# Optimization experiments

Measured on AMD Instinct MI355X. Metric: run time of the kernel, lower is better.

The kernel has to match this reference:

```python
import jax, jax.numpy as jnp
import numpy as np

B, TV, TH, F, H, D = 16, 128, 64, 512, 512, 256


def setup_inputs() -> dict:
    key = jax.random.key(0)
    ks = jax.random.split(key, 6)
    return {
        "v": jax.random.normal(ks[0], (B, TV, F), dtype=jnp.float32),
        "h": jax.random.normal(ks[1], (B, TH, H), dtype=jnp.float32),
        "W": jax.random.normal(ks[2], (F, D), dtype=jnp.float32) * 0.05,
        "U": jax.random.normal(ks[3], (H, D), dtype=jnp.float32) * 0.05,
        "b": jax.random.normal(ks[4], (D,), dtype=jnp.float32) * 0.05,
        "w": jax.random.normal(ks[5], (D, 1), dtype=jnp.float32) * 0.05,
    }


def reference(v, h, W, U, b, w):
    # v: [B, Tv, F] video features; h: [B, Th, H] decoder hidden states
    Wv = jnp.einsum("btf,fd->btd", v, W)      # [B, Tv, D]
    Uh = jnp.einsum("bsh,hd->bsd", h, U)      # [B, Th, D]
    # Broadcast add -> [B, Th, Tv, D], tanh nonlinearity (additive attention)
    f = jnp.tanh(Uh[:, :, None, :] + Wv[:, None, :, :] + b)
    q = jnp.einsum("bstd,d->bst", f, w[:, 0])  # scores [B, Th, Tv]
    beta = jax.nn.softmax(q, axis=-1)           # softmax over Tv (axis -2 of q[..., None])
    u = jnp.einsum("bst,btf->bsf", beta, v)    # context [B, Th, F]
    return u
```

## Files before the change

### kernel.cpp

```cpp
#include <hip/hip_runtime.h>
#include <hip/hip_bf16.h>

#define BB 16
#define TV 128
#define TH 64
#define FF 512
#define HH 512
#define DD 256

#define LOG2E2 2.8853900817779268f

typedef __attribute__((ext_vector_type(8))) short bf16x8;
typedef __attribute__((ext_vector_type(4))) float f32x4;

__device__ __forceinline__ float fast_exp2(float x) {
#if __has_builtin(__builtin_amdgcn_exp2f)
  return __builtin_amdgcn_exp2f(x);
#else
  return __expf(x * 0.6931471805599453f);
#endif
}
__device__ __forceinline__ float fast_rcp(float x) {
#if __has_builtin(__builtin_amdgcn_rcpf)
  return __builtin_amdgcn_rcpf(x);
#else
  return 1.0f / x;
#endif
}
__device__ __forceinline__ unsigned short f2bf(float x) {
  union { float f; unsigned u; } a; a.f = x;
  unsigned r = a.u + 0x7fffu + ((a.u >> 16) & 1u);
  return (unsigned short)(r >> 16);
}

#define NT_V 262144
#define NT_H 131072
#define NT_W 32768
__global__ __launch_bounds__(256) void convert_kernel(
    const float* __restrict__ v, const float* __restrict__ h,
    const float* __restrict__ W, const float* __restrict__ U,
    unsigned short* __restrict__ vb, unsigned short* __restrict__ hb,
    unsigned short* __restrict__ WT, unsigned short* __restrict__ UT) {
  int task = blockIdx.x * 256 + threadIdx.x;
  if (task < NT_V) {
    float4 x = ((const float4*)v)[task];
    ushort4 o = make_ushort4(f2bf(x.x), f2bf(x.y), f2bf(x.z), f2bf(x.w));
    *(ushort4*)&vb[(size_t)task * 4] = o;
  } else if (task < NT_V + NT_H) {
    int t2 = task - NT_V;
    float4 x = ((const float4*)h)[t2];
    ushort4 o = make_ushort4(f2bf(x.x), f2bf(x.y), f2bf(x.z), f2bf(x.w));
    *(ushort4*)&hb[(size_t)t2 * 4] = o;
  } else {
    int t2 = task - NT_V - NT_H;
    const float* S;
    unsigned short* Dt;
    if (t2 < NT_W) { S = W; Dt = WT; } else { S = U; Dt = UT; t2 -= NT_W; }
    int n = t2 & 255, k4 = t2 >> 8;
    float a0 = S[(k4 * 4 + 0) * 256 + n];
    float a1 = S[(k4 * 4 + 1) * 256 + n];
    float a2 = S[(k4 * 4 + 2) * 256 + n];
    float a3 = S[(k4 * 4 + 3) * 256 + n];
    ushort4 o = make_ushort4(f2bf(a0), f2bf(a1), f2bf(a2), f2bf(a3));
    *(ushort4*)&Dt[(size_t)n * 512 + k4 * 4] = o;
  }
}

__global__ __launch_bounds__(128) void mfma_gemm_kernel(
    const unsigned short* __restrict__ Av, const unsigned short* __restrict__ Ah,
    const unsigned short* __restrict__ WT, const unsigned short* __restrict__ UT,
    const float* __restrict__ bias, float* __restrict__ EaT,
    float* __restrict__ EuhT) {
  const int bid = blockIdx.x;
  const unsigned short* A;
  const unsigned short* BT;
  int mt, nt;
  bool is_wv;
  if (bid < 256) {
    A = Av; BT = WT; is_wv = true;
    mt = bid >> 3; nt = bid & 7;
  } else {
    const int b2 = bid - 256;
    A = Ah; BT = UT; is_wv = false;
    mt = b2 >> 3; nt = b2 & 7;
  }
  const int wv   = threadIdx.x >> 6;
  const int lane = threadIdx.x & 63;
  const int m0   = mt * 64 + wv * 32;
  const int n0   = nt * 32;
  const int r16  = lane & 15;
  const int quad = lane >> 4;

  const unsigned short* a0p = A + (size_t)(m0 + r16) * 512 + quad * 8;
  const unsigned short* a1p = a0p + 16 * 512;
  const unsigned short* b0p = BT + (size_t)(n0 + r16) * 512 + quad * 8;
  const unsigned short* b1p = b0p + 16 * 512;

  f32x4 acc00 = {0.f, 0.f, 0.f, 0.f};
  f32x4 acc01 = {0.f, 0.f, 0.f, 0.f};
  f32x4 acc10 = {0.f, 0.f, 0.f, 0.f};
  f32x4 acc11 = {0.f, 0.f, 0.f, 0.f};

#pragma unroll
  for (int kc = 0; kc < 16; kc++) {
    bf16x8 a0 = *(const bf16x8*)(a0p + kc * 32);
    bf16x8 a1 = *(const bf16x8*)(a1p + kc * 32);
    bf16x8 b0 = *(const bf16x8*)(b0p + kc * 32);
    bf16x8 b1 = *(const bf16x8*)(b1p + kc * 32);
    acc00 = __builtin_amdgcn_mfma_f32_16x16x32_bf16(a0, b0, acc00, 0, 0, 0);
    acc01 = __builtin_amdgcn_mfma_f32_16x16x32_bf16(a0, b1, acc01, 0, 0, 0);
    acc10 = __builtin_amdgcn_mfma_f32_16x16x32_bf16(a1, b0, acc10, 0, 0, 0);
    acc11 = __builtin_amdgcn_mfma_f32_16x16x32_bf16(a1, b1, acc11, 0, 0, 0);
  }

  if (is_wv) {
    const int bb   = m0 >> 7;
    const int tb   = (m0 & 127) + quad * 4;
    float* Wb = EaT + (size_t)bb * 32768;
#pragma unroll
    for (int r = 0; r < 4; r++) {
      Wb[(size_t)(n0 + r16) * 128 + tb + r]           = fast_exp2(acc00[r] * LOG2E2);
      Wb[(size_t)(n0 + 16 + r16) * 128 + tb + r]      = fast_exp2(acc01[r] * LOG2E2);
      Wb[(size_t)(n0 + r16) * 128 + tb + 16 + r]      = fast_exp2(acc10[r] * LOG2E2);
      Wb[(size_t)(n0 + 16 + r16) * 128 + tb + 16 + r] = fast_exp2(acc11[r] * LOG2E2);
    }
  } else {
    const float bj0 = bias[n0 + r16];
    const float bj1 = bias[n0 + 16 + r16];
#pragma unroll
    for (int r = 0; r < 4; r++) {
      const int row0 = m0 + quad * 4 + r;
      EuhT[(size_t)row0 * 256 + n0 + r16]             = fast_exp2((acc00[r] + bj0) * LOG2E2);
      EuhT[(size_t)row0 * 256 + n0 + 16 + r16]        = fast_exp2((acc01[r] + bj1) * LOG2E2);
      EuhT[(size_t)(row0 + 16) * 256 + n0 + r16]      = fast_exp2((acc10[r] + bj0) * LOG2E2);
      EuhT[(size_t)(row0 + 16) * 256 + n0 + 16 + r16] = fast_exp2((acc11[r] + bj1) * LOG2E2);
    }
  }
}

__global__ __launch_bounds__(1024) void attn_fused_kernel(
    const float* __restrict__ EaT, const float* __restrict__ EuhT,
    const float* __restrict__ wg, const float* __restrict__ v,
    float* __restrict__ u) {
  __shared__ float EuhS[4 * 256];
  __shared__ float wS[256];
  __shared__ float pS[4 * 16 * 128];
  __shared__ float bS[4 * 128];
  __shared__ float mW[8];
  __shared__ float sW[8];

  const int tid = threadIdx.x;
  const int bid  = blockIdx.x;
  const int slot = bid >> 3;
  const int b    = (bid & 7) * 2 + (slot >> 4);
  const int sg   = slot & 15;
  const int s0   = sg * 4;

  if (tid < 256) {
    const int row = tid >> 6, q4 = (tid & 63) << 2;
    *(float4*)&EuhS[row * 256 + q4] =
        *(const float4*)&EuhT[(size_t)(b * 64 + s0 + row) * 256 + q4];
  } else if (tid < 320) {
    const int q4 = (tid - 256) << 2;
    *(float4*)&wS[q4] = *(const float4*)&wg[q4];
  }
  __syncthreads();

  {
    const int t4  = tid & 31;
    const int dgf = tid >> 5;
    const float* eab = EaT + (size_t)b * 32768 + (size_t)dgf * 8 * 128 + t4 * 4;

    float eu[4][8];
    float wr[8];
#pragma unroll
    for (int s = 0; s < 4; s++) {
      *(float4*)&eu[s][0] = *(const float4*)&EuhS[s * 256 + dgf * 8];
      *(float4*)&eu[s][4] = *(const float4*)&EuhS[s * 256 + dgf * 8 + 4];
    }
    *(float4*)&wr[0] = *(const float4*)&wS[dgf * 8];
    *(float4*)&wr[4] = *(const float4*)&wS[dgf * 8 + 4];

    f32x4 acc[4];
#pragma unroll
    for (int s = 0; s < 4; s++) acc[s] = (f32x4){0.f, 0.f, 0.f, 0.f};

#pragma unroll
    for (int jp = 0; jp < 4; jp++) {
      float4 e0 = *(const float4*)(eab + (2 * jp + 0) * 128);
      float4 e1 = *(const float4*)(eab + (2 * jp + 1) * 128);
      const float w0 = wr[2 * jp], w1 = wr[2 * jp + 1];
#pragma unroll
      for (int s = 0; s < 4; s++) {
        const float u0 = eu[s][2 * jp], u1 = eu[s][2 * jp + 1];
        float D0, D1, num;
        D0 = fmaf(e0.x, u0, 1.0f); D1 = fmaf(e1.x, u1, 1.0f);
        num = fmaf(w1, D0, w0 * D1);
        acc[s][0] = fmaf(num, fast_rcp(D0 * D1), acc[s][0]);
        D0 = fmaf(e0.y, u0, 1.0f); D1 = fmaf(e1.y, u1, 1.0f);
        num = fmaf(w1, D0, w0 * D1);
        acc[s][1] = fmaf(num, fast_rcp(D0 * D1), acc[s][1]);
        D0 = fmaf(e0.z, u0, 1.0f); D1 = fmaf(e1.z, u1, 1.0f);
        num = fmaf(w1, D0, w0 * D1);
        acc[s][2] = fmaf(num, fast_rcp(D0 * D1), acc[s][2]);
        D0 = fmaf(e0.w, u0, 1.0f); D1 = fmaf(e1.w, u1, 1.0f);
        num = fmaf(w1, D0, w0 * D1);
        acc[s][3] = fmaf(num, fast_rcp(D0 * D1), acc[s][3]);
      }
    }

#pragma unroll
    for (int s = 0; s < 4; s++) {
#pragma unroll
      for (int c = 0; c < 4; c++) acc[s][c] += __shfl_xor(acc[s][c], 32, 64);
    }
    const int wv_ = tid >> 6;
    if ((tid & 63) < 32) {
#pragma unroll
      for (int s = 0; s < 4; s++) {
        float4 o = make_float4(acc[s][0], acc[s][1], acc[s][2], acc[s][3]);
        *(float4*)&pS[(s * 16 + wv_) * 128 + t4 * 4] = o;
      }
    }
  }
  __syncthreads();

  float qv = 0.0f, ev = 0.0f;
  const int wvid = tid >> 6, lane = tid & 63;
  if (tid < 512) {
    const int s_l = tid >> 7, t = tid & 127;
    float ssum = 0.0f;
#pragma unroll
    for (int k = 0; k < 16; k++) ssum += pS[(s_l * 16 + k) * 128 + t];
    qv = ssum * (-LOG2E2);
    float m = qv;
#pragma unroll
    for (int off = 32; off > 0; off >>= 1) m = fmaxf(m, __shfl_xor(m, off, 64));
    if (lane == 0) mW[wvid] = m;
  }
  __syncthreads();
  if (tid < 512) {
    float m = fmaxf(mW[wvid], mW[wvid ^ 1]);
    ev = fast_exp2(qv - m);
    float ssum = ev;
#pragma unroll
    for (int off = 32; off > 0; off >>= 1) ssum += __shfl_xor(ssum, off, 64);
    if (lane == 0) sW[wvid] = ssum;
  }
  __syncthreads();
  if (tid < 512) {
    const int s_l = tid >> 7, t = tid & 127;
    bS[s_l * 128 + t] = ev * fast_rcp(sW[wvid] + sW[wvid ^ 1]);
  }
  __syncthreads();

  const float* vb2 = v + (size_t)b * TV * FF;
  const int f  = tid & 511;
  const int sh = tid >> 9;
  float a0 = 0.f, a1 = 0.f;
#pragma unroll 4
  for (int tg = 0; tg < 128; tg += 4) {
    float4 b0 = *(const float4*)&bS[(sh * 2 + 0) * 128 + tg];
    float4 b1 = *(const float4*)&bS[(sh * 2 + 1) * 128 + tg];
    float v0 = vb2[(tg + 0) * 512 + f];
    float v1 = vb2[(tg + 1) * 512 + f];
    float v2 = vb2[(tg + 2) * 512 + f];
    float v3 = vb2[(tg + 3) * 512 + f];
    a0 = fmaf(b0.x, v0, a0); a0 = fmaf(b0.y, v1, a0);
    a0 = fmaf(b0.z, v2, a0); a0 = fmaf(b0.w, v3, a0);
    a1 = fmaf(b1.x, v0, a1); a1 = fmaf(b1.y, v1, a1);
    a1 = fmaf(b1.z, v2, a1); a1 = fmaf(b1.w, v3, a1);
  }
  float* urow = u + (size_t)(b * 64 + s0 + sh * 2) * 512;
  urow[0 * 512 + f] = a0;
  urow[1 * 512 + f] = a1;
}

extern "C" void kernel_launch(void* const* d_in, const int* in_sizes, int n_in,
                              void* d_out, int out_size, void* d_ws, size_t ws_size,
                              hipStream_t stream) {
  const float* v  = (const float*)d_in[0];
  const float* h  = (const float*)d_in[1];
  const float* W  = (const float*)d_in[2];
  const float* U  = (const float*)d_in[3];
  const float* bb = (const float*)d_in[4];
  const float* w  = (const float*)d_in[5];
  float* u = (float*)d_out;

  float* EaT  = (float*)d_ws;
  float* EuhT = EaT + (size_t)2048 * 256;
  unsigned short* vb16 = (unsigned short*)(EuhT + (size_t)1024 * 256);
  unsigned short* hb16 = vb16 + (size_t)2048 * 512;
  unsigned short* WT   = hb16 + (size_t)1024 * 512;
  unsigned short* UT   = WT + (size_t)256 * 512;

  convert_kernel<<<1792, 256, 0, stream>>>(v, h, W, U, vb16, hb16, WT, UT);
  mfma_gemm_kernel<<<384, 128, 0, stream>>>(vb16, hb16, WT, UT, bb, EaT, EuhT);
  attn_fused_kernel<<<256, 1024, 0, stream>>>(EaT, EuhT, w, v, u);
}
```

Baseline: 90.78 us.

## Fuse fp32-to-bf16 activation conversion into GEMM and split context reduction over time

The GEMM kernel now reads fp32 v and h directly and converts them to bf16 in registers, so the separate conversion pass and its bf16 staging buffers go away. Only W and U are still transposed and converted in a small kernel. The GEMM tile becomes one wave computing 32x64, which gives more B reuse per A load but fewer threads per block. In the attention kernel, the context product splits the time axis between the two thread halves, each accumulating four rows, and the halves are combined through shared memory. This halves each thread's v reads and adds a barrier plus a shared-memory reduction.

Result: no change. 91.13 us (+0.4%).

```diff
diff --git a/kernel.cpp b/kernel.cpp
--- a/kernel.cpp
+++ b/kernel.cpp
@@ -33,107 +33,118 @@
   return (unsigned short)(r >> 16);
 }
 
-#define NT_V 262144
-#define NT_H 131072
-#define NT_W 32768
-__global__ __launch_bounds__(256) void convert_kernel(
-    const float* __restrict__ v, const float* __restrict__ h,
+__device__ __forceinline__ bf16x8 cvt8(const float4 x, const float4 y) {
+  union { bf16x8 v; unsigned short e[8]; } r;
+  r.e[0] = f2bf(x.x); r.e[1] = f2bf(x.y); r.e[2] = f2bf(x.z); r.e[3] = f2bf(x.w);
+  r.e[4] = f2bf(y.x); r.e[5] = f2bf(y.y); r.e[6] = f2bf(y.z); r.e[7] = f2bf(y.w);
+  return r.v;
+}
+
+__global__ __launch_bounds__(256) void convert_wu_kernel(
     const float* __restrict__ W, const float* __restrict__ U,
-    unsigned short* __restrict__ vb, unsigned short* __restrict__ hb,
     unsigned short* __restrict__ WT, unsigned short* __restrict__ UT) {
-  int task = blockIdx.x * 256 + threadIdx.x;
-  if (task < NT_V) {
-    float4 x = ((const float4*)v)[task];
-    ushort4 o = make_ushort4(f2bf(x.x), f2bf(x.y), f2bf(x.z), f2bf(x.w));
-    *(ushort4*)&vb[(size_t)task * 4] = o;
-  } else if (task < NT_V + NT_H) {
-    int t2 = task - NT_V;
-    float4 x = ((const float4*)h)[t2];
-    ushort4 o = make_ushort4(f2bf(x.x), f2bf(x.y), f2bf(x.z), f2bf(x.w));
-    *(ushort4*)&hb[(size_t)t2 * 4] = o;
-  } else {
-    int t2 = task - NT_V - NT_H;
-    const float* S;
-    unsigned short* Dt;
-    if (t2 < NT_W) { S = W; Dt = WT; } else { S = U; Dt = UT; t2 -= NT_W; }
-    int n = t2 & 255, k4 = t2 >> 8;
-    float a0 = S[(k4 * 4 + 0) * 256 + n];
-    float a1 = S[(k4 * 4 + 1) * 256 + n];
-    float a2 = S[(k4 * 4 + 2) * 256 + n];
-    float a3 = S[(k4 * 4 + 3) * 256 + n];
-    ushort4 o = make_ushort4(f2bf(a0), f2bf(a1), f2bf(a2), f2bf(a3));
-    *(ushort4*)&Dt[(size_t)n * 512 + k4 * 4] = o;
-  }
-}
-
-__global__ __launch_bounds__(128) void mfma_gemm_kernel(
-    const unsigned short* __restrict__ Av, const unsigned short* __restrict__ Ah,
+  int t2 = blockIdx.x * 256 + threadIdx.x;
+  const float* S;
+  unsigned short* Dt;
+  if (t2 < 32768) { S = W; Dt = WT; } else { S = U; Dt = UT; t2 -= 32768; }
+  int n = t2 & 255, k4 = t2 >> 8;
+  float a0 = S[(k4 * 4 + 0) * 256 + n];
+  float a1 = S[(k4 * 4 + 1) * 256 + n];
+  float a2 = S[(k4 * 4 + 2) * 256 + n];
+  float a3 = S[(k4 * 4 + 3) * 256 + n];
+  ushort4 o = make_ushort4(f2bf(a0), f2bf(a1), f2bf(a2), f2bf(a3));
+  *(ushort4*)&Dt[(size_t)n * 512 + k4 * 4] = o;
+}
+
+__global__ __launch_bounds__(64) void mfma_gemm_kernel(
+    const float* __restrict__ Av, const float* __restrict__ Ah,
     const unsigned short* __restrict__ WT, const unsigned short* __restrict__ UT,
     const float* __restrict__ bias, float* __restrict__ EaT,
     float* __restrict__ EuhT) {
   const int bid = blockIdx.x;
-  const unsigned short* A;
+  const float* A;
   const unsigned short* BT;
   int mt, nt;
   bool is_wv;
   if (bid < 256) {
     A = Av; BT = WT; is_wv = true;
-    mt = bid >> 3; nt = bid & 7;
+    mt = bid >> 2; nt = bid & 3;
   } else {
     const int b2 = bid - 256;
     A = Ah; BT = UT; is_wv = false;
-    mt = b2 >> 3; nt = b2 & 7;
-  }
-  const int wv   = threadIdx.x >> 6;
+    mt = b2 >> 2; nt = b2 & 3;
+  }
   const int lane = threadIdx.x & 63;
-  const int m0   = mt * 64 + wv * 32;
-  const int n0   = nt * 32;
+  const int m0   = mt * 32;
+  const int n0   = nt * 64;
   const int r16  = lane & 15;
   const int quad = lane >> 4;
 
-  const unsigned short* a0p = A + (size_t)(m0 + r16) * 512 + quad * 8;
-  const unsigned short* a1p = a0p + 16 * 512;
-  const unsigned short* b0p = BT + (size_t)(n0 + r16) * 512 + quad * 8;
-  const unsigned short* b1p = b0p + 16 * 512;
-
-  f32x4 acc00 = {0.f, 0.f, 0.f, 0.f};
-  f32x4 acc01 = {0.f, 0.f, 0.f, 0.f};
-  f32x4 acc10 = {0.f, 0.f, 0.f, 0.f};
-  f32x4 acc11 = {0.f, 0.f, 0.f, 0.f};
+  const float* a0p = A + (size_t)(m0 + r16) * 512 + quad * 8;
+  const float* a1p = a0p + 16 * 512;
+  const unsigned short* bp0 = BT + (size_t)(n0 + r16) * 512 + quad * 8;
+  const unsigned short* bp1 = bp0 + 16 * 512;
+  const unsigned short* bp2 = bp0 + 32 * 512;
+  const unsigned short* bp3 = bp0 + 48 * 512;
+
+  f32x4 acc[2][4];
+#pragma unroll
+  for (int i = 0; i < 2; i++)
+#pragma unroll
+    for (int j = 0; j < 4; j++) acc[i][j] = (f32x4){0.f, 0.f, 0.f, 0.f};
 
 #pragma unroll
   for (int kc = 0; kc < 16; kc++) {
-    bf16x8 a0 = *(const bf16x8*)(a0p + kc * 32);
-    bf16x8 a1 = *(const bf16x8*)(a1p + kc * 32);
-    bf16x8 b0 = *(const bf16x8*)(b0p + kc * 32);
-    bf16x8 b1 = *(const bf16x8*)(b1p + kc * 32);
-    acc00 = __builtin_amdgcn_mfma_f32_16x16x32_bf16(a0, b0, acc00, 0, 0, 0);
-    acc01 = __builtin_amdgcn_mfma_f32_16x16x32_bf16(a0, b1, acc01, 0, 0, 0);
-    acc10 = __builtin_amdgcn_mfma_f32_16x16x32_bf16(a1, b0, acc10, 0, 0, 0);
-    acc11 = __builtin_amdgcn_mfma_f32_16x16x32_bf16(a1, b1, acc11, 0, 0, 0);
+    float4 a0lo = *(const float4*)(a0p + kc * 32);
+    float4 a0hi = *(const float4*)(a0p + kc * 32 + 4);
+    float4 a1lo = *(const float4*)(a1p + kc * 32);
+    float4 a1hi = *(const float4*)(a1p + kc * 32 + 4);
+    bf16x8 fa0 = cvt8(a0lo, a0hi);
+    bf16x8 fa1 = cvt8(a1lo, a1hi);
+    bf16x8 fb0 = *(const bf16x8*)(bp0 + kc * 32);
+    bf16x8 fb1 = *(const bf16x8*)(bp1 + kc * 32);
+    bf16x8 fb2 = *(const bf16x8*)(bp2 + kc * 32);
+    bf16x8 fb3 = *(const bf16x8*)(bp3 + kc * 32);
+    acc[0][0] = __builtin_amdgcn_mfma_f32_16x16x32_bf16(fa0, fb0, acc[0][0], 0, 0, 0);
+    acc[0][1] = __builtin_amdgcn_mfma_f32_16x16x32_bf16(fa0, fb1, acc[0][1], 0, 0, 0);
+    acc[0][2] = __builtin_amdgcn_mfma_f32_16x16x32_bf16(fa0, fb2, acc[0][2], 0, 0, 0);
+    acc[0][3] = __builtin_amdgcn_mfma_f32_16x16x32_bf16(fa0, fb3, acc[0][3], 0, 0, 0);
+    acc[1][0] = __builtin_amdgcn_mfma_f32_16x16x32_bf16(fa1, fb0, acc[1][0], 0, 0, 0);
+    acc[1][1] = __builtin_amdgcn_mfma_f32_16x16x32_bf16(fa1, fb1, acc[1][1], 0, 0, 0);
+    acc[1][2] = __builtin_amdgcn_mfma_f32_16x16x32_bf16(fa1, fb2, acc[1][2], 0, 0, 0);
+    acc[1][3] = __builtin_amdgcn_mfma_f32_16x16x32_bf16(fa1, fb3, acc[1][3], 0, 0, 0);
   }
 
   if (is_wv) {
-    const int bb   = m0 >> 7;
-    const int tb   = (m0 & 127) + quad * 4;
+    const int bb = m0 >> 7;
+    const int tb = (m0 & 127) + quad * 4;
     float* Wb = EaT + (size_t)bb * 32768;
 #pragma unroll
-    for (int r = 0; r < 4; r++) {
-      Wb[(size_t)(n0 + r16) * 128 + tb + r]           = fast_exp2(acc00[r] * LOG2E2);
-      Wb[(size_t)(n0 + 16 + r16) * 128 + tb + r]      = fast_exp2(acc01[r] * LOG2E2);
-      Wb[(size_t)(n0 + r16) * 128 + tb + 16 + r]      = fast_exp2(acc10[r] * LOG2E2);
-      Wb[(size_t)(n0 + 16 + r16) * 128 + tb + 16 + r] = fast_exp2(acc11[r] * LOG2E2);
+    for (int i = 0; i < 2; i++) {
+#pragma unroll
+      for (int j = 0; j < 4; j++) {
+#pragma unroll
+        for (int r = 0; r < 4; r++) {
+          Wb[(size_t)(n0 + 16 * j + r16) * 128 + tb + 16 * i + r] =
+              fast_exp2(acc[i][j][r] * LOG2E2);
+        }
+      }
     }
   } else {
-    const float bj0 = bias[n0 + r16];
-    const float bj1 = bias[n0 + 16 + r16];
-#pragma unroll
-    for (int r = 0; r < 4; r++) {
-      const int row0 = m0 + quad * 4 + r;
-      EuhT[(size_t)row0 * 256 + n0 + r16]             = fast_exp2((acc00[r] + bj0) * LOG2E2);
-      EuhT[(size_t)row0 * 256 + n0 + 16 + r16]        = fast_exp2((acc01[r] + bj1) * LOG2E2);
-      EuhT[(size_t)(row0 + 16) * 256 + n0 + r16]      = fast_exp2((acc10[r] + bj0) * LOG2E2);
-      EuhT[(size_t)(row0 + 16) * 256 + n0 + 16 + r16] = fast_exp2((acc11[r] + bj1) * LOG2E2);
+    float bj[4];
+#pragma unroll
+    for (int j = 0; j < 4; j++) bj[j] = bias[n0 + 16 * j + r16];
+#pragma unroll
+    for (int i = 0; i < 2; i++) {
+#pragma unroll
+      for (int j = 0; j < 4; j++) {
+#pragma unroll
+        for (int r = 0; r < 4; r++) {
+          const int row = m0 + 16 * i + quad * 4 + r;
+          EuhT[(size_t)row * 256 + n0 + 16 * j + r16] =
+              fast_exp2((acc[i][j][r] + bj[j]) * LOG2E2);
+        }
+      }
     }
   }
 }
@@ -254,14 +265,17 @@
   }
   __syncthreads();
 
-  const float* vb2 = v + (size_t)b * TV * FF;
   const int f  = tid & 511;
-  const int sh = tid >> 9;
-  float a0 = 0.f, a1 = 0.f;
+  const int th = tid >> 9;
+  const float* vb2 = v + (size_t)b * TV * FF + (size_t)th * 64 * FF;
+  const float* bsp = &bS[th * 64];
+  float a0 = 0.f, a1 = 0.f, a2 = 0.f, a3 = 0.f;
 #pragma unroll 4
-  for (int tg = 0; tg < 128; tg += 4) {
-    float4 b0 = *(const float4*)&bS[(sh * 2 + 0) * 128 + tg];
-    float4 b1 = *(const float4*)&bS[(sh * 2 + 1) * 128 + tg];
+  for (int tg = 0; tg < 64; tg += 4) {
+    float4 b0 = *(const float4*)&bsp[0 * 128 + tg];
+    float4 b1 = *(const float4*)&bsp[1 * 128 + tg];
+    float4 b2 = *(const float4*)&bsp[2 * 128 + tg];
+    float4 b3 = *(const float4*)&bsp[3 * 128 + tg];
     float v0 = vb2[(tg + 0) * 512 + f];
     float v1 = vb2[(tg + 1) * 512 + f];
     float v2 = vb2[(tg + 2) * 512 + f];
@@ -270,10 +284,26 @@
     a0 = fmaf(b0.z, v2, a0); a0 = fmaf(b0.w, v3, a0);
     a1 = fmaf(b1.x, v0, a1); a1 = fmaf(b1.y, v1, a1);
     a1 = fmaf(b1.z, v2, a1); a1 = fmaf(b1.w, v3, a1);
-  }
-  float* urow = u + (size_t)(b * 64 + s0 + sh * 2) * 512;
-  urow[0 * 512 + f] = a0;
-  urow[1 * 512 + f] = a1;
+    a2 = fmaf(b2.x, v0, a2); a2 = fmaf(b2.y, v1, a2);
+    a2 = fmaf(b2.z, v2, a2); a2 = fmaf(b2.w, v3, a2);
+    a3 = fmaf(b3.x, v0, a3); a3 = fmaf(b3.y, v1, a3);
+    a3 = fmaf(b3.z, v2, a3); a3 = fmaf(b3.w, v3, a3);
+  }
+  float* uP = pS;
+  uP[(th * 4 + 0) * 512 + f] = a0;
+  uP[(th * 4 + 1) * 512 + f] = a1;
+  uP[(th * 4 + 2) * 512 + f] = a2;
+  uP[(th * 4 + 3) * 512 + f] = a3;
+  __syncthreads();
+  {
+    int oi = tid;
+#pragma unroll
+    for (int rep = 0; rep < 2; rep++, oi += 1024) {
+      const int s = oi >> 9, ff = oi & 511;
+      const float val = uP[s * 512 + ff] + uP[(s + 4) * 512 + ff];
+      u[(size_t)(b * 64 + s0 + s) * 512 + ff] = val;
+    }
+  }
 }
 
 extern "C" void kernel_launch(void* const* d_in, const int* in_sizes, int n_in,
@@ -289,12 +319,10 @@
 
   float* EaT  = (float*)d_ws;
   float* EuhT = EaT + (size_t)2048 * 256;
-  unsigned short* vb16 = (unsigned short*)(EuhT + (size_t)1024 * 256);
-  unsigned short* hb16 = vb16 + (size_t)2048 * 512;
-  unsigned short* WT   = hb16 + (size_t)1024 * 512;
-  unsigned short* UT   = WT + (size_t)256 * 512;
-
-  convert_kernel<<<1792, 256, 0, stream>>>(v, h, W, U, vb16, hb16, WT, UT);
-  mfma_gemm_kernel<<<384, 128, 0, stream>>>(vb16, hb16, WT, UT, bb, EaT, EuhT);
+  unsigned short* WT = (unsigned short*)(EuhT + (size_t)1024 * 256);
+  unsigned short* UT = WT + (size_t)256 * 512;
+
+  convert_wu_kernel<<<256, 256, 0, stream>>>(W, U, WT, UT);
+  mfma_gemm_kernel<<<384, 64, 0, stream>>>(v, h, WT, UT, bb, EaT, EuhT);
   attn_fused_kernel<<<256, 1024, 0, stream>>>(EaT, EuhT, w, v, u);
 }
```
